# Performance work log

Measured on AMD Instinct MI355X. Metric: run time of the kernel, lower is better.

The kernel has to match this reference:

```python
import jax, jax.numpy as jnp
import numpy as np

N = 500_000      # total observations
D = 40           # per-observation feature dim
S = 2048         # number of segments (time series)
WIDTH = 128      # psi hidden width
LATENT = 128     # latent width
DOT = 64         # dot_prod_dim
HEADS = 4        # n_heads


def setup_inputs() -> dict:
    key = jax.random.key(0)
    ks = jax.random.split(key, 12)

    def he(k, shape):
        fan_in = shape[0]
        lim = np.sqrt(6.0 / fan_in)
        return jax.random.uniform(k, shape, jnp.float32, -lim, lim)

    inputs = jax.random.normal(ks[0], (N, D), jnp.float32)
    segment_ids = jnp.sort(jax.random.randint(ks[1], (N,), 0, S))
    lengths = jax.random.randint(ks[2], (S,), 0, 300)
    return {
        "inputs": inputs,
        "segment_ids": segment_ids,
        "lengths": lengths,
        "W1": he(ks[3], (D, WIDTH)),      "b1": jnp.zeros((WIDTH,), jnp.float32),
        "W2": he(ks[4], (WIDTH, WIDTH)), "b2": jnp.zeros((WIDTH,), jnp.float32),
        "W3": he(ks[5], (WIDTH, LATENT)),"b3": jnp.zeros((LATENT,), jnp.float32),
        "Wr": he(ks[6], (LATENT, LATENT)),"br": jnp.zeros((LATENT,), jnp.float32),
        "W_k": he(ks[7], (LATENT + D, DOT * HEADS)),
        "W_q": jax.random.normal(ks[8], (HEADS, DOT), jnp.float32) * 0.02,
    }


def segment_softmax(x, seg, num_segments):
    # x: [N, H]; softmax over elements sharing the same segment id
    m = jax.ops.segment_max(x, seg, num_segments, indices_are_sorted=True)
    e = jnp.exp(x - m[seg])
    denom = jax.ops.segment_sum(e, seg, num_segments, indices_are_sorted=True)
    return e / denom[seg]


def reference(inputs, segment_ids, lengths, W1, b1, W2, b2, W3, b3, Wr, br, W_k, W_q):
    relu = jax.nn.relu
    # psi: 2 hidden dense layers + latent projection (all relu)
    h = relu(inputs @ W1 + b1)
    h = relu(h @ W2 + b2)
    enc = relu(h @ W3 + b3)                                   # [N, LATENT]
    # segment mean aggregation
    sums = jax.ops.segment_sum(enc, segment_ids, S, indices_are_sorted=True)
    counts = jax.ops.segment_sum(jnp.ones((enc.shape[0], 1), enc.dtype),
                                 segment_ids, S, indices_are_sorted=True)
    agg = sums / jnp.maximum(counts, 1.0)                      # [S, LATENT]
    agg = relu(agg @ Wr + br)                                  # rho
    # broadcast back and combine
    combined = jnp.concatenate([inputs, agg[segment_ids]], axis=-1)  # [N, D+LATENT]
    keys = (combined @ W_k).reshape(-1, HEADS, DOT)            # split+stack == reshape
    preattn = jnp.einsum('nhd,hd->nh', keys, W_q) / jnp.sqrt(jnp.float32(DOT))
    attn = segment_softmax(preattn, segment_ids, S)            # [N, H]
    # match original: list of per-head [N, 1] tensors -> stacked [H, N, 1]
    return jnp.transpose(attn)[..., None]
```

## Files before the change

kernel.cpp:

```cpp
#include <hip/hip_runtime.h>
#include <math.h>


#define NROWS 500000
#define DIM 40
#define NSEG 2048
#define DOTD 64
#define NH 4
#define BLOCK 256
#define NWAVE (BLOCK / 64)
#define CACHE_ROWS 512

__global__ __launch_bounds__(BLOCK) void prep_kernel(
    const int* __restrict__ seg,
    const float* __restrict__ Wk,
    const float* __restrict__ Wq,
    int* __restrict__ seg_start,
    int* __restrict__ seg_end,
    float* __restrict__ wxg)
{
    const int tid = (int)threadIdx.x;
    const int n = (int)(blockIdx.x * BLOCK + tid);

    if (blockIdx.x == 0 && tid < DIM * NH) {
        const int d = tid >> 2;
        const int h = tid & 3;
        const float* wkp = Wk + d * (NH * DOTD) + h * DOTD;
        const float* wqp = Wq + h * DOTD;
        float acc = 0.f;
        #pragma unroll
        for (int j = 0; j < DOTD; ++j) acc += wkp[j] * wqp[j];
        wxg[tid] = acc * 0.125f;
    }

    if (n < NROWS) {
        const int s = seg[n];
        if (n == 0) {
            seg_start[s] = 0;
            for (int t = 0; t < s; ++t) { seg_start[t] = 0; seg_end[t] = 0; }
        } else {
            const int sp = seg[n - 1];
            if (sp != s) {
                seg_start[s] = n;
                seg_end[sp] = n;
                for (int t = sp + 1; t < s; ++t) { seg_start[t] = n; seg_end[t] = n; }
            }
        }
        if (n == NROWS - 1) {
            seg_end[s] = NROWS;
            for (int t = s + 1; t < NSEG; ++t) { seg_start[t] = NROWS; seg_end[t] = NROWS; }
        }
    }
}

__device__ __forceinline__ void compute_logits(
    const float* __restrict__ x, int n, const float (*wx)[NH], float* acc)
{
    const float4* xr = (const float4*)(x + (size_t)n * DIM);
    #pragma unroll
    for (int h = 0; h < NH; ++h) acc[h] = 0.f;
    #pragma unroll
    for (int q = 0; q < DIM / 4; ++q) {
        const float4 v = xr[q];
        #pragma unroll
        for (int h = 0; h < NH; ++h) {
            acc[h] += v.x * wx[4 * q + 0][h];
            acc[h] += v.y * wx[4 * q + 1][h];
            acc[h] += v.z * wx[4 * q + 2][h];
            acc[h] += v.w * wx[4 * q + 3][h];
        }
    }
}

__global__ __launch_bounds__(BLOCK) void seg_attn_kernel(
    const float* __restrict__ x,
    const int* __restrict__ seg_start,
    const int* __restrict__ seg_end,
    const float* __restrict__ wxg,
    float* __restrict__ out)
{
    __shared__ float wx[DIM][NH];
    __shared__ float red_max[NWAVE][NH];
    __shared__ float red_sum[NWAVE][NH];
    __shared__ float cache_l[NH][CACHE_ROWS];

    const int tid = (int)threadIdx.x;
    if (tid < DIM * NH) wx[tid >> 2][tid & 3] = wxg[tid];

    const int s = (int)blockIdx.x;
    const int start = seg_start[s];
    const int rows = seg_end[s] - start;
    __syncthreads();
    if (rows <= 0) return;

    const int lane = tid & 63;
    const int wid = tid >> 6;
    const int iters = (rows + BLOCK - 1) / BLOCK;

    float lmax[NH];
    #pragma unroll
    for (int h = 0; h < NH; ++h) lmax[h] = -3.0e38f;

    for (int it = 0; it < iters; ++it) {
        const int i = it * BLOCK + tid;
        if (i < rows) {
            float acc[NH];
            compute_logits(x, start + i, wx, acc);
            if (i < CACHE_ROWS) {
                #pragma unroll
                for (int h = 0; h < NH; ++h) cache_l[h][i] = acc[h];
            }
            #pragma unroll
            for (int h = 0; h < NH; ++h) lmax[h] = fmaxf(lmax[h], acc[h]);
        }
    }

    #pragma unroll
    for (int h = 0; h < NH; ++h) {
        float v = lmax[h];
        #pragma unroll
        for (int off = 32; off > 0; off >>= 1) v = fmaxf(v, __shfl_xor(v, off, 64));
        if (lane == 0) red_max[wid][h] = v;
    }
    __syncthreads();
    float m[NH];
    #pragma unroll
    for (int h = 0; h < NH; ++h)
        m[h] = fmaxf(fmaxf(red_max[0][h], red_max[1][h]),
                     fmaxf(red_max[2][h], red_max[3][h]));

    float lsum[NH] = {0.f, 0.f, 0.f, 0.f};
    for (int it = 0; it < iters; ++it) {
        const int i = it * BLOCK + tid;
        if (i < rows) {
            float acc[NH];
            if (i < CACHE_ROWS) {
                #pragma unroll
                for (int h = 0; h < NH; ++h) acc[h] = cache_l[h][i];
            } else {
                compute_logits(x, start + i, wx, acc);
            }
            #pragma unroll
            for (int h = 0; h < NH; ++h) lsum[h] += __expf(acc[h] - m[h]);
        }
    }

    #pragma unroll
    for (int h = 0; h < NH; ++h) {
        float v = lsum[h];
        #pragma unroll
        for (int off = 32; off > 0; off >>= 1) v += __shfl_xor(v, off, 64);
        if (lane == 0) red_sum[wid][h] = v;
    }
    __syncthreads();
    float rden[NH];
    #pragma unroll
    for (int h = 0; h < NH; ++h)
        rden[h] = 1.0f / (red_sum[0][h] + red_sum[1][h] +
                          red_sum[2][h] + red_sum[3][h]);

    for (int it = 0; it < iters; ++it) {
        const int i = it * BLOCK + tid;
        if (i < rows) {
            float acc[NH];
            if (i < CACHE_ROWS) {
                #pragma unroll
                for (int h = 0; h < NH; ++h) acc[h] = cache_l[h][i];
            } else {
                compute_logits(x, start + i, wx, acc);
            }
            const int n = start + i;
            #pragma unroll
            for (int h = 0; h < NH; ++h)
                out[(size_t)h * NROWS + n] = __expf(acc[h] - m[h]) * rden[h];
        }
    }
}

extern "C" void kernel_launch(void* const* d_in, const int* in_sizes, int n_in,
                              void* d_out, int out_size, void* d_ws, size_t ws_size,
                              hipStream_t stream) {
    const float* x  = (const float*)d_in[0];
    const int* seg  = (const int*)d_in[1];
    const float* Wk = (const float*)d_in[11];
    const float* Wq = (const float*)d_in[12];
    float* out = (float*)d_out;

    int* seg_start = (int*)d_ws;
    int* seg_end   = seg_start + NSEG;
    float* wxg     = (float*)(seg_end + NSEG);

    hipLaunchKernelGGL(prep_kernel, dim3((NROWS + BLOCK - 1) / BLOCK), dim3(BLOCK),
                       0, stream, seg, Wk, Wq, seg_start, seg_end, wxg);
    hipLaunchKernelGGL(seg_attn_kernel, dim3(NSEG), dim3(BLOCK),
                       0, stream, x, seg_start, seg_end, wxg, out);
}
```

Baseline: 170.7 us.

## Use one wavefront per segment with four rows per lane and cached exponentials

The segment softmax kernel now launches a single 64-lane wavefront per segment instead of a 256-thread block. Each lane processes four rows per pass, which removes the cross-wave shared-memory reductions and the barriers between phases. The projected weights are stored head-major so they can be read as float4, and the cache keeps exp values so the final pass only has to multiply. The cost is fewer threads per segment (about 244 rows per segment on average), so each lane does more serial work, latency hiding depends on having many blocks resident, and the wide accumulators raise register pressure.

Measured after the change: 218.6 us. 1.28x slower.

```diff
diff --git a/kernel.cpp b/kernel.cpp
--- a/kernel.cpp
+++ b/kernel.cpp
@@ -4,14 +4,15 @@
 
 #define NROWS 500000
 #define DIM 40
+#define NQ (DIM / 4)
 #define NSEG 2048
 #define DOTD 64
 #define NH 4
-#define BLOCK 256
-#define NWAVE (BLOCK / 64)
+#define PBLOCK 256
 #define CACHE_ROWS 512
-
-__global__ __launch_bounds__(BLOCK) void prep_kernel(
+#define RPL 4
+
+__global__ __launch_bounds__(PBLOCK) void prep_kernel(
     const int* __restrict__ seg,
     const float* __restrict__ Wk,
     const float* __restrict__ Wq,
@@ -20,17 +21,17 @@
     float* __restrict__ wxg)
 {
     const int tid = (int)threadIdx.x;
-    const int n = (int)(blockIdx.x * BLOCK + tid);
+    const int n = (int)(blockIdx.x * PBLOCK + tid);
 
     if (blockIdx.x == 0 && tid < DIM * NH) {
-        const int d = tid >> 2;
-        const int h = tid & 3;
+        const int h = tid / DIM;
+        const int d = tid - h * DIM;
         const float* wkp = Wk + d * (NH * DOTD) + h * DOTD;
         const float* wqp = Wq + h * DOTD;
         float acc = 0.f;
         #pragma unroll
         for (int j = 0; j < DOTD; ++j) acc += wkp[j] * wqp[j];
-        wxg[tid] = acc * 0.125f;
+        wxg[h * DIM + d] = acc * 0.125f;
     }
 
     if (n < NROWS) {
@@ -53,126 +54,149 @@
     }
 }
 
-__device__ __forceinline__ void compute_logits(
-    const float* __restrict__ x, int n, const float (*wx)[NH], float* acc)
+__device__ __forceinline__ void recompute_logits(
+    const float4* __restrict__ x4, const float (*wxl)[DIM], int n, float* a)
 {
-    const float4* xr = (const float4*)(x + (size_t)n * DIM);
-    #pragma unroll
-    for (int h = 0; h < NH; ++h) acc[h] = 0.f;
-    #pragma unroll
-    for (int q = 0; q < DIM / 4; ++q) {
-        const float4 v = xr[q];
+    #pragma unroll
+    for (int h = 0; h < NH; ++h) a[h] = 0.f;
+    #pragma unroll
+    for (int q = 0; q < NQ; ++q) {
+        const float4 v = x4[(size_t)n * NQ + q];
         #pragma unroll
         for (int h = 0; h < NH; ++h) {
-            acc[h] += v.x * wx[4 * q + 0][h];
-            acc[h] += v.y * wx[4 * q + 1][h];
-            acc[h] += v.z * wx[4 * q + 2][h];
-            acc[h] += v.w * wx[4 * q + 3][h];
-        }
-    }
-}
-
-__global__ __launch_bounds__(BLOCK) void seg_attn_kernel(
+            const float4 w = ((const float4*)wxl[h])[q];
+            a[h] += v.x * w.x + v.y * w.y + v.z * w.z + v.w * w.w;
+        }
+    }
+}
+
+__global__ __launch_bounds__(64) void seg_attn_kernel(
     const float* __restrict__ x,
     const int* __restrict__ seg_start,
     const int* __restrict__ seg_end,
     const float* __restrict__ wxg,
     float* __restrict__ out)
 {
-    __shared__ float wx[DIM][NH];
-    __shared__ float red_max[NWAVE][NH];
-    __shared__ float red_sum[NWAVE][NH];
-    __shared__ float cache_l[NH][CACHE_ROWS];
-
-    const int tid = (int)threadIdx.x;
-    if (tid < DIM * NH) wx[tid >> 2][tid & 3] = wxg[tid];
-
+    __shared__ __align__(16) float wxl[NH][DIM];
+    __shared__ float cache[NH][CACHE_ROWS];
+
+    const int lane = (int)threadIdx.x;
     const int s = (int)blockIdx.x;
     const int start = seg_start[s];
     const int rows = seg_end[s] - start;
+    if (rows <= 0) return;
+
+    {
+        float* wf = &wxl[0][0];
+        for (int t = lane; t < NH * DIM; t += 64) wf[t] = wxg[t];
+    }
     __syncthreads();
-    if (rows <= 0) return;
-
-    const int lane = tid & 63;
-    const int wid = tid >> 6;
-    const int iters = (rows + BLOCK - 1) / BLOCK;
+
+    const float4* x4 = (const float4*)x;
+    const int sup = (rows + 255) >> 8;
 
     float lmax[NH];
     #pragma unroll
     for (int h = 0; h < NH; ++h) lmax[h] = -3.0e38f;
 
-    for (int it = 0; it < iters; ++it) {
-        const int i = it * BLOCK + tid;
-        if (i < rows) {
-            float acc[NH];
-            compute_logits(x, start + i, wx, acc);
-            if (i < CACHE_ROWS) {
+    for (int si = 0; si < sup; ++si) {
+        const int base = (si << 8) + lane;
+        float acc[RPL][NH];
+        #pragma unroll
+        for (int k = 0; k < RPL; ++k)
+            #pragma unroll
+            for (int h = 0; h < NH; ++h) acc[k][h] = 0.f;
+
+        #pragma unroll
+        for (int q = 0; q < NQ; ++q) {
+            float4 w[NH];
+            #pragma unroll
+            for (int h = 0; h < NH; ++h) w[h] = ((const float4*)wxl[h])[q];
+            #pragma unroll
+            for (int k = 0; k < RPL; ++k) {
+                const int i = base + (k << 6);
+                if (i < rows) {
+                    const float4 v = x4[(size_t)(start + i) * NQ + q];
+                    #pragma unroll
+                    for (int h = 0; h < NH; ++h)
+                        acc[k][h] += v.x * w[h].x + v.y * w[h].y
+                                   + v.z * w[h].z + v.w * w[h].w;
+                }
+            }
+        }
+        #pragma unroll
+        for (int k = 0; k < RPL; ++k) {
+            const int i = base + (k << 6);
+            if (i < rows) {
                 #pragma unroll
-                for (int h = 0; h < NH; ++h) cache_l[h][i] = acc[h];
-            }
-            #pragma unroll
-            for (int h = 0; h < NH; ++h) lmax[h] = fmaxf(lmax[h], acc[h]);
-        }
-    }
-
+                for (int h = 0; h < NH; ++h) {
+                    if (i < CACHE_ROWS) cache[h][i] = acc[k][h];
+                    lmax[h] = fmaxf(lmax[h], acc[k][h]);
+                }
+            }
+        }
+    }
+
+    float m[NH];
     #pragma unroll
     for (int h = 0; h < NH; ++h) {
         float v = lmax[h];
         #pragma unroll
         for (int off = 32; off > 0; off >>= 1) v = fmaxf(v, __shfl_xor(v, off, 64));
-        if (lane == 0) red_max[wid][h] = v;
-    }
-    __syncthreads();
-    float m[NH];
-    #pragma unroll
-    for (int h = 0; h < NH; ++h)
-        m[h] = fmaxf(fmaxf(red_max[0][h], red_max[1][h]),
-                     fmaxf(red_max[2][h], red_max[3][h]));
+        m[h] = v;
+    }
 
     float lsum[NH] = {0.f, 0.f, 0.f, 0.f};
-    for (int it = 0; it < iters; ++it) {
-        const int i = it * BLOCK + tid;
-        if (i < rows) {
-            float acc[NH];
-            if (i < CACHE_ROWS) {
-                #pragma unroll
-                for (int h = 0; h < NH; ++h) acc[h] = cache_l[h][i];
-            } else {
-                compute_logits(x, start + i, wx, acc);
-            }
-            #pragma unroll
-            for (int h = 0; h < NH; ++h) lsum[h] += __expf(acc[h] - m[h]);
-        }
-    }
-
+    for (int si = 0; si < sup; ++si) {
+        const int base = (si << 8) + lane;
+        #pragma unroll
+        for (int k = 0; k < RPL; ++k) {
+            const int i = base + (k << 6);
+            if (i < rows) {
+                if (i < CACHE_ROWS) {
+                    #pragma unroll
+                    for (int h = 0; h < NH; ++h) {
+                        const float e = __expf(cache[h][i] - m[h]);
+                        cache[h][i] = e;
+                        lsum[h] += e;
+                    }
+                } else {
+                    float a[NH];
+                    recompute_logits(x4, wxl, start + i, a);
+                    #pragma unroll
+                    for (int h = 0; h < NH; ++h) lsum[h] += __expf(a[h] - m[h]);
+                }
+            }
+        }
+    }
+    float rden[NH];
     #pragma unroll
     for (int h = 0; h < NH; ++h) {
         float v = lsum[h];
         #pragma unroll
         for (int off = 32; off > 0; off >>= 1) v += __shfl_xor(v, off, 64);
-        if (lane == 0) red_sum[wid][h] = v;
-    }
-    __syncthreads();
-    float rden[NH];
-    #pragma unroll
-    for (int h = 0; h < NH; ++h)
-        rden[h] = 1.0f / (red_sum[0][h] + red_sum[1][h] +
-                          red_sum[2][h] + red_sum[3][h]);
-
-    for (int it = 0; it < iters; ++it) {
-        const int i = it * BLOCK + tid;
-        if (i < rows) {
-            float acc[NH];
-            if (i < CACHE_ROWS) {
-                #pragma unroll
-                for (int h = 0; h < NH; ++h) acc[h] = cache_l[h][i];
-            } else {
-                compute_logits(x, start + i, wx, acc);
-            }
-            const int n = start + i;
-            #pragma unroll
-            for (int h = 0; h < NH; ++h)
-                out[(size_t)h * NROWS + n] = __expf(acc[h] - m[h]) * rden[h];
+        rden[h] = 1.0f / v;
+    }
+
+    for (int si = 0; si < sup; ++si) {
+        const int base = (si << 8) + lane;
+        #pragma unroll
+        for (int k = 0; k < RPL; ++k) {
+            const int i = base + (k << 6);
+            if (i < rows) {
+                const int n = start + i;
+                if (i < CACHE_ROWS) {
+                    #pragma unroll
+                    for (int h = 0; h < NH; ++h)
+                        out[(size_t)h * NROWS + n] = cache[h][i] * rden[h];
+                } else {
+                    float a[NH];
+                    recompute_logits(x4, wxl, n, a);
+                    #pragma unroll
+                    for (int h = 0; h < NH; ++h)
+                        out[(size_t)h * NROWS + n] = __expf(a[h] - m[h]) * rden[h];
+                }
+            }
         }
     }
 }
@@ -190,8 +214,8 @@
     int* seg_end   = seg_start + NSEG;
     float* wxg     = (float*)(seg_end + NSEG);
 
-    hipLaunchKernelGGL(prep_kernel, dim3((NROWS + BLOCK - 1) / BLOCK), dim3(BLOCK),
+    hipLaunchKernelGGL(prep_kernel, dim3((NROWS + PBLOCK - 1) / PBLOCK), dim3(PBLOCK),
                        0, stream, seg, Wk, Wq, seg_start, seg_end, wxg);
-    hipLaunchKernelGGL(seg_attn_kernel, dim3(NSEG), dim3(BLOCK),
+    hipLaunchKernelGGL(seg_attn_kernel, dim3(NSEG), dim3(64),
                        0, stream, x, seg_start, seg_end, wxg, out);
 }
```
